# Kernel optimization log

Hardware: AMD Instinct MI355X
Metric: run time of the kernel (lower is better)

The kernel has to match this reference:

```python
import jax, jax.numpy as jnp
import numpy as np

N_SAMPLES = 8192
EMBED_DIM = 128
NUM_CLASSES = 100


def setup_inputs() -> dict:
    key = jax.random.key(0)
    k1, k2 = jax.random.split(key)
    x = jax.random.normal(k1, (N_SAMPLES, EMBED_DIM), dtype=jnp.float32)
    # FastAP assumes L2-normalized embeddings (dist2 = 2 - 2*cos in [0, 4])
    x = x / jnp.linalg.norm(x, axis=1, keepdims=True)
    labels = jax.random.randint(k2, (N_SAMPLES,), 0, NUM_CLASSES, dtype=jnp.int64 if jax.config.jax_enable_x64 else jnp.int32)
    return {"batch": x, "labels": labels, "num_bins": 10}


def reference(batch, labels, num_bins):
    N = batch.shape[0]
    L = num_bins + 1                      # number of histogram bin centers (edges of linspace)
    Delta = 4.0 / num_bins                # bin width
    Z = jnp.linspace(0.0, 4.0, L)

    same = labels[:, None] == labels[None, :]
    eye = jnp.eye(N, dtype=bool)
    I_pos = (same & ~eye).astype(batch.dtype)   # Aff > 0
    I_neg = (~same).astype(batch.dtype)         # Aff < 0 (diag is 'same', so excluded)
    N_pos = I_pos.sum(axis=1)

    # squared euclidean distance for unit-norm rows: 2 - 2*cos
    dist2 = 2.0 - 2.0 * (batch @ batch.T)       # [N, N]

    # soft-binning histogram: one N x N pulse per bin, reduced to per-row counts.
    # lax.map keeps only one [N, N] pulse buffer alive at a time.
    def bin_fn(z):
        pulse = jnp.maximum(0.0, 1.0 - jnp.abs(dist2 - z) / Delta)
        return (jnp.einsum('ij,ij->i', pulse, I_pos),
                jnp.einsum('ij,ij->i', pulse, I_neg))

    hp, hn = jax.lax.map(bin_fn, Z)             # each [L, N]
    h_pos = hp.T                                # [N, L]
    h_neg = hn.T

    H_pos = jnp.cumsum(h_pos, axis=1)
    H = jnp.cumsum(h_pos + h_neg, axis=1)

    # FastAP = h_pos * H_pos / H, with NaN/Inf (H == 0) zeroed, as in the original
    safe_H = jnp.where(H > 0, H, 1.0)
    ap = jnp.where(H > 0, h_pos * H_pos / safe_H, 0.0).sum(axis=1)

    # divide by N_pos; rows with no positives are dropped from the mean
    valid = N_pos > 0
    safe_Np = jnp.where(valid, N_pos, 1.0)
    ap = jnp.where(valid, ap / safe_Np, 0.0)

    n_valid = valid.sum().astype(batch.dtype)
    loss = 1.0 - ap.sum() / n_valid
    return loss
```

## Files before the change

### kernel.cpp

```cpp
#include <hip/hip_runtime.h>

#define NS 8192
#define EMBED 128
#define ROWCHUNK 512
#define NPANEL (ROWCHUNK / 32)
#define AROW 12
#define INV64K (1.0f / 65536.0f)
#define NCLS 100
#define NCAP 160

typedef __bf16 bf16x8 __attribute__((ext_vector_type(8)));
typedef float f32x4 __attribute__((ext_vector_type(4)));
typedef float f32x2 __attribute__((ext_vector_type(2)));
typedef const __attribute__((address_space(1))) unsigned ag_u32;
typedef __attribute__((address_space(3))) unsigned al_u32;

#define OFF_XB  0u
#define OFF_GS  2097152u
#define OFF_GA  4194304u
#define OFF_POS 4587520u
#define OFF_AC  4980736u
#define ZERO_BYTES 786448u

__device__ inline unsigned short f2bf(float f) {
  unsigned u = __float_as_uint(f);
  u += 0x7fffu + ((u >> 16) & 1u);
  return (unsigned short)(u >> 16);
}
__device__ inline float clamp01(float x) { return __builtin_amdgcn_fmed3f(x, 0.f, 1.f); }

__global__ __launch_bounds__(256) void prep_kernel(const float* __restrict__ x,
                                                   unsigned short* __restrict__ xb,
                                                   uint4* __restrict__ zbase) {
  const int gid = blockIdx.x * 256 + threadIdx.x;
  const int row = gid >> 4, g = gid & 15;
  const float4 v0 = reinterpret_cast<const float4*>(x)[row * 32 + g * 2];
  const float4 v1 = reinterpret_cast<const float4*>(x)[row * 32 + g * 2 + 1];
  uint4 o;
  o.x = (unsigned)f2bf(v0.x) | ((unsigned)f2bf(v0.y) << 16);
  o.y = (unsigned)f2bf(v0.z) | ((unsigned)f2bf(v0.w) << 16);
  o.z = (unsigned)f2bf(v1.x) | ((unsigned)f2bf(v1.y) << 16);
  o.w = (unsigned)f2bf(v1.z) | ((unsigned)f2bf(v1.w) << 16);
  reinterpret_cast<uint4*>(xb)[row * 16 + (g ^ (row & 7))] = o;
  if (gid < (int)(ZERO_BYTES / 16u)) zbase[gid] = make_uint4(0u, 0u, 0u, 0u);
}

__global__ __launch_bounds__(256, 8) void fastap_main_kernel(
    const unsigned short* __restrict__ xb,
    const int* __restrict__ labels,
    float* __restrict__ gS, unsigned* __restrict__ gA,
    float* __restrict__ gPos) {
  __shared__ __align__(16) unsigned short sA[2][32 * 128];
  __shared__ int sList[NCAP];
  __shared__ int sCnt;

  const int tid  = threadIdx.x;
  const int wave = tid >> 6;
  const int lane = tid & 63;
  const int l16  = lane & 15;
  const int quad = lane >> 4;

  if (blockIdx.y == NS / ROWCHUNK) {
    if (blockIdx.x >= NCLS) return;
    const int cls = blockIdx.x;

    if (tid == 0) sCnt = 0;
    __syncthreads();
    for (int base = wave * 64; base < NS; base += 256) {
      const int lab = labels[base + lane];
      const unsigned long long m = __ballot(lab == cls);
      if (m) {
        const int fl = (int)__builtin_ctzll(m);
        int wb = 0;
        if (lane == fl) wb = atomicAdd(&sCnt, (int)__popcll(m));
        wb = __shfl(wb, fl, 64);
        if (lab == cls) {
          const int rank = (int)__popcll(m & ((1ull << lane) - 1ull));
          const int idx = wb + rank;
          if (idx < NCAP) sList[idx] = base + lane;
        }
      }
    }
    __syncthreads();
    const int nc = min(sCnt, NCAP);

    for (int cT = wave * 16; cT < nc; cT += 64) {
      const int sc = cT + l16;
      const int Rc = sList[(sc < nc) ? sc : cT];
      bf16x8 bfr[4];
      #pragma unroll
      for (int kb = 0; kb < 4; ++kb) {
        const int pg = (kb * 4 + quad) ^ (Rc & 7);
        bfr[kb] = *reinterpret_cast<const bf16x8*>(&xb[Rc * 128 + pg * 8]);
      }

      f32x2 Hp0 = {0.f, 0.f}, Hp1 = {0.f, 0.f}, Hp2 = {0.f, 0.f};
      f32x2 Hp3 = {0.f, 0.f}, Hp4 = {0.f, 0.f};
      float Hp10 = 0.f;

      for (int rT = 0; rT < nc; rT += 16) {
        const int rl = rT + l16;
        const int Rr = sList[(rl < nc) ? rl : rT];
        f32x4 acc = {0.f, 0.f, 0.f, 0.f};
        #pragma unroll
        for (int kb = 0; kb < 4; ++kb) {
          const int pg = (kb * 4 + quad) ^ (Rr & 7);
          const bf16x8 afr =
              *reinterpret_cast<const bf16x8*>(&xb[Rr * 128 + pg * 8]);
          acc = __builtin_amdgcn_mfma_f32_16x16x32_bf16(afr, bfr[kb], acc, 0, 0, 0);
        }
        #pragma unroll
        for (int r = 0; r < 4; ++r) {
          const int row = rT + quad * 4 + r;
          if (row == sc || row >= nc) continue;
          const float a = acc[r];
          const f32x2 av = {a, a};
          f32x2 t;
          t = __builtin_elementwise_fma(av, (f32x2){5.f, 5.f}, (f32x2){-4.f, -3.f});
          Hp0 += (f32x2){clamp01(t.x), clamp01(t.y)};
          t = __builtin_elementwise_fma(av, (f32x2){5.f, 5.f}, (f32x2){-2.f, -1.f});
          Hp1 += (f32x2){clamp01(t.x), clamp01(t.y)};
          t = __builtin_elementwise_fma(av, (f32x2){5.f, 5.f}, (f32x2){0.f, 1.f});
          Hp2 += (f32x2){clamp01(t.x), clamp01(t.y)};
          t = __builtin_elementwise_fma(av, (f32x2){5.f, 5.f}, (f32x2){2.f, 3.f});
          Hp3 += (f32x2){clamp01(t.x), clamp01(t.y)};
          t = __builtin_elementwise_fma(av, (f32x2){5.f, 5.f}, (f32x2){4.f, 5.f});
          Hp4 += (f32x2){clamp01(t.x), clamp01(t.y)};
          Hp10 += clamp01(fmaf(a, 5.f, 6.f));
        }
      }

      #pragma unroll
      for (int m = 16; m < 64; m <<= 1) {
        Hp0.x += __shfl_xor(Hp0.x, m, 64); Hp0.y += __shfl_xor(Hp0.y, m, 64);
        Hp1.x += __shfl_xor(Hp1.x, m, 64); Hp1.y += __shfl_xor(Hp1.y, m, 64);
        Hp2.x += __shfl_xor(Hp2.x, m, 64); Hp2.y += __shfl_xor(Hp2.y, m, 64);
        Hp3.x += __shfl_xor(Hp3.x, m, 64); Hp3.y += __shfl_xor(Hp3.y, m, 64);
        Hp4.x += __shfl_xor(Hp4.x, m, 64); Hp4.y += __shfl_xor(Hp4.y, m, 64);
        Hp10  += __shfl_xor(Hp10,  m, 64);
      }

      if (quad == 0 && sc < nc) {
        float4* gp = reinterpret_cast<float4*>(gPos + sList[sc] * 12);
        gp[0] = make_float4(Hp0.x, Hp0.y, Hp1.x, Hp1.y);
        gp[1] = make_float4(Hp2.x, Hp2.y, Hp3.x, Hp3.y);
        gp[2] = make_float4(Hp4.x, Hp4.y, Hp10, (float)(nc - 1));
      }
    }
    return;
  }

  const int colBase  = blockIdx.x * 64;
  const int rowChunk = blockIdx.y * ROWCHUNK;

  const int jcol = colBase + wave * 16 + l16;
  bf16x8 bfr[4];
  #pragma unroll
  for (int kb = 0; kb < 4; ++kb) {
    const int pg = (kb * 4 + quad) ^ (l16 & 7);
    bfr[kb] = *reinterpret_cast<const bf16x8*>(&xb[jcol * 128 + pg * 8]);
  }

  f32x2 C01 = {0.f, 0.f}, C23 = {0.f, 0.f};

  int aOff[4];
  #pragma unroll
  for (int kb = 0; kb < 4; ++kb)
    aOff[kb] = l16 * 128 + (((kb * 4 + quad) ^ (l16 & 7)) << 3);

  const unsigned short* xrb = xb + rowChunk * 128;
  auto stage = [&](int p, int b) {
    const unsigned short* src = xrb + p * (32 * 128);
    __builtin_amdgcn_global_load_lds((ag_u32*)(src + tid * 8),
                                     (al_u32*)(&sA[b][tid * 8]), 16, 0, 0);
    __builtin_amdgcn_global_load_lds((ag_u32*)(src + (tid + 256) * 8),
                                     (al_u32*)(&sA[b][(tid + 256) * 8]), 16, 0, 0);
  };

  auto tile16 = [&](const unsigned short* ap, int lcr) {
    bf16x8 a0 = *reinterpret_cast<const bf16x8*>(&ap[aOff[0]]);
    bf16x8 a1 = *reinterpret_cast<const bf16x8*>(&ap[aOff[1]]);
    bf16x8 a2 = *reinterpret_cast<const bf16x8*>(&ap[aOff[2]]);
    bf16x8 a3 = *reinterpret_cast<const bf16x8*>(&ap[aOff[3]]);
    f32x4 acc = {0.f, 0.f, 0.f, 0.f};
    acc = __builtin_amdgcn_mfma_f32_16x16x32_bf16(a0, bfr[0], acc, 0, 0, 0);
    acc = __builtin_amdgcn_mfma_f32_16x16x32_bf16(a1, bfr[1], acc, 0, 0, 0);
    acc = __builtin_amdgcn_mfma_f32_16x16x32_bf16(a2, bfr[2], acc, 0, 0, 0);
    acc = __builtin_amdgcn_mfma_f32_16x16x32_bf16(a3, bfr[3], acc, 0, 0, 0);

    #pragma unroll
    for (int r = 0; r < 4; ++r) {
      const float a = acc[r];
      const f32x2 av = {a, a};
      f32x2 d01 = __builtin_elementwise_fma(av, (f32x2){5.f, 5.f},
                                            (f32x2){-1.f, 0.f});
      f32x2 d23 = __builtin_elementwise_fma(av, (f32x2){5.f, 5.f},
                                            (f32x2){1.f, 2.f});
      d01 = (f32x2){clamp01(d01.x), clamp01(d01.y)};
      d23 = (f32x2){clamp01(d23.x), clamp01(d23.y)};
      C01 += d01; C23 += d23;
    }

    const float mabs = fmaxf(fmaxf(fabsf(acc[0]), fabsf(acc[1])),
                             fmaxf(fabsf(acc[2]), fabsf(acc[3])));
    if (__builtin_expect(mabs > 0.4f, 0)) {
      #pragma unroll
      for (int r = 0; r < 4; ++r) {
        const float a = acc[r];
        if (fabsf(a) <= 0.4f) continue;
        const int i = rowChunk + lcr + quad * 4 + r;
        const float d0 = clamp01(fmaf(a, 5.f, -1.f));
        const float d1 = clamp01(a * 5.f);
        const float d2 = clamp01(fmaf(a, 5.f, 1.f));
        const float d3 = clamp01(fmaf(a, 5.f, 2.f));
        if (i == jcol) {
          C01 -= (f32x2){d0, d1};  C23 -= (f32x2){d2, d3};
          #pragma unroll
          for (int k = 7; k <= 10; ++k)
            atomicAdd(&gA[jcol * AROW + k], (unsigned)(-65536));
        } else {
          const float t = fmaf(a, -5.f, 5.f);
          #pragma unroll
          for (int k = 0; k <= 2; ++k) {
            const float v = clamp01((float)(k + 1) - t);
            const int q = (int)(v * 65536.f + 0.5f);
            if (q) atomicAdd(&gA[jcol * AROW + k], (unsigned)q);
          }
          #pragma unroll
          for (int k = 7; k <= 10; ++k) {
            const float v = clamp01((float)(k + 1) - t) - 1.f;
            const int q = (int)(v * 65536.f - 0.5f);
            if (q) atomicAdd(&gA[jcol * AROW + k], (unsigned)q);
          }
        }
      }
    }
  };

  stage(0, 0);
  __syncthreads();

  #pragma unroll 1
  for (int p = 0; p < NPANEL; ++p) {
    const int cur = p & 1;
    if (p + 1 < NPANEL) stage(p + 1, cur ^ 1);
    tile16(&sA[cur][0],        p * 32);
    tile16(&sA[cur][16 * 128], p * 32 + 16);
    __syncthreads();
  }

  #pragma unroll
  for (int m = 16; m < 64; m <<= 1) {
    C01.x += __shfl_xor(C01.x, m, 64); C01.y += __shfl_xor(C01.y, m, 64);
    C23.x += __shfl_xor(C23.x, m, 64); C23.y += __shfl_xor(C23.y, m, 64);
  }

  if (quad == 0) {
    const int slot = blockIdx.y;
    const float4 cv = make_float4(C01.x, C01.y, C23.x, C23.y);
    reinterpret_cast<float4*>(gS)[slot * NS + jcol] = cv;
  }
}

__global__ __launch_bounds__(256) void epilogue_kernel(
    const float* __restrict__ gS, const unsigned* __restrict__ gA,
    const float* __restrict__ gPos,
    float* __restrict__ accum, unsigned* __restrict__ done,
    float* __restrict__ out) {
  const int i = blockIdx.x * 256 + threadIdx.x;
  const float4* gS4 = reinterpret_cast<const float4*>(gS);
  float4 Cs = make_float4(0.f, 0.f, 0.f, 0.f);
  #pragma unroll 4
  for (int c = 0; c < 16; ++c) {
    const float4 u = gS4[c * NS + i];
    Cs.x += u.x; Cs.y += u.y; Cs.z += u.z; Cs.w += u.w;
  }
  const float CsA[4] = {Cs.x, Cs.y, Cs.z, Cs.w};

  const float4* gp4 = reinterpret_cast<const float4*>(gPos + i * 12);
  const float4 h0 = gp4[0], h1 = gp4[1], h2 = gp4[2];
  const float Hp[11] = {h0.x, h0.y, h0.z, h0.w, h1.x, h1.y,
                        h1.z, h1.w, h2.x, h2.y, h2.z};
  const int np = (int)h2.w;

  float ap = 0.f, val = 0.f, HpPrev = 0.f;
  #pragma unroll
  for (int b = 0; b <= 10; ++b) {
    const float baseH = (b < 3) ? 0.f : (b < 7) ? CsA[b - 3] : 8192.f;
    const float H = baseH + (float)(int)gA[i * AROW + b] * INV64K;
    const float hp = Hp[b] - HpPrev;
    HpPrev = Hp[b];
    if (H > 1e-6f) ap += hp * Hp[b] / H;
  }
  if (np > 0) { ap /= (float)np; val = 1.f; } else ap = 0.f;

  __shared__ float sa[256], sv[256];
  sa[threadIdx.x] = ap; sv[threadIdx.x] = val;
  __syncthreads();
  for (int s = 128; s > 0; s >>= 1) {
    if (threadIdx.x < s) {
      sa[threadIdx.x] += sa[threadIdx.x + s];
      sv[threadIdx.x] += sv[threadIdx.x + s];
    }
    __syncthreads();
  }
  if (threadIdx.x == 0) {
    atomicAdd(&accum[0], sa[0]);
    atomicAdd(&accum[1], sv[0]);
    __threadfence();
    const unsigned prev = atomicAdd(done, 1u);
    if (prev == gridDim.x - 1) {
      const float a = atomicAdd(&accum[0], 0.f);
      const float c = atomicAdd(&accum[1], 0.f);
      out[0] = 1.f - (c > 0.f ? a / c : 0.f);
    }
  }
}

extern "C" void kernel_launch(void* const* d_in, const int* in_sizes, int n_in,
                              void* d_out, int out_size, void* d_ws, size_t ws_size,
                              hipStream_t stream) {
  const float* x      = (const float*)d_in[0];
  const int*   labels = (const int*)d_in[1];
  float* out = (float*)d_out;

  char* ws = (char*)d_ws;
  unsigned short* xb = (unsigned short*)(ws + OFF_XB);
  float*    gS    = (float*)(ws + OFF_GS);
  unsigned* gA    = (unsigned*)(ws + OFF_GA);
  float*    gPos  = (float*)(ws + OFF_POS);
  float*    accum = (float*)(ws + OFF_AC);
  unsigned* done  = (unsigned*)(ws + OFF_AC + 8);

  prep_kernel<<<512, 256, 0, stream>>>(x, xb, (uint4*)(ws + OFF_GA));
  fastap_main_kernel<<<dim3(NS / 64, NS / ROWCHUNK + 1), 256, 0, stream>>>(
      xb, labels, gS, gA, gPos);
  epilogue_kernel<<<NS / 256, 256, 0, stream>>>(gS, gA, gPos, accum, done, out);
}
```

Baseline: 107.6 us.

## Retile waves to 2x2 MFMA tiles sharing A fragments across two column groups

```diff
diff --git a/kernel.cpp b/kernel.cpp
--- a/kernel.cpp
+++ b/kernel.cpp
@@ -17,9 +17,9 @@
 
 #define OFF_XB  0u
 #define OFF_GS  2097152u
-#define OFF_GA  4194304u
-#define OFF_POS 4587520u
-#define OFF_AC  4980736u
+#define OFF_GA  6291456u
+#define OFF_POS 6684672u
+#define OFF_AC  7077888u
 #define ZERO_BYTES 786448u
 
 __device__ inline unsigned short f2bf(float f) {
@@ -150,23 +150,32 @@
     return;
   }
 
+  const int w2   = wave >> 1;
+  const int wr   = wave & 1;
   const int colBase  = blockIdx.x * 64;
   const int rowChunk = blockIdx.y * ROWCHUNK;
 
-  const int jcol = colBase + wave * 16 + l16;
-  bf16x8 bfr[4];
+  bf16x8 bfr[2][4];
+  int jcolv[2];
   #pragma unroll
-  for (int kb = 0; kb < 4; ++kb) {
-    const int pg = (kb * 4 + quad) ^ (l16 & 7);
-    bfr[kb] = *reinterpret_cast<const bf16x8*>(&xb[jcol * 128 + pg * 8]);
-  }
-
-  f32x2 C01 = {0.f, 0.f}, C23 = {0.f, 0.f};
+  for (int s = 0; s < 2; ++s) {
+    const int jc = colBase + w2 * 32 + s * 16 + l16;
+    jcolv[s] = jc;
+    #pragma unroll
+    for (int kb = 0; kb < 4; ++kb) {
+      const int pg = (kb * 4 + quad) ^ (l16 & 7);
+      bfr[s][kb] = *reinterpret_cast<const bf16x8*>(&xb[jc * 128 + pg * 8]);
+    }
+  }
+
+  f32x2 C01[2], C23[2];
+  C01[0] = (f32x2){0.f, 0.f}; C23[0] = (f32x2){0.f, 0.f};
+  C01[1] = (f32x2){0.f, 0.f}; C23[1] = (f32x2){0.f, 0.f};
 
   int aOff[4];
   #pragma unroll
   for (int kb = 0; kb < 4; ++kb)
-    aOff[kb] = l16 * 128 + (((kb * 4 + quad) ^ (l16 & 7)) << 3);
+    aOff[kb] = (wr * 16 + l16) * 128 + (((kb * 4 + quad) ^ (l16 & 7)) << 3);
 
   const unsigned short* xrb = xb + rowChunk * 128;
   auto stage = [&](int p, int b) {
@@ -177,60 +186,74 @@
                                      (al_u32*)(&sA[b][(tid + 256) * 8]), 16, 0, 0);
   };
 
-  auto tile16 = [&](const unsigned short* ap, int lcr) {
+  auto panel32 = [&](const unsigned short* ap, int p) {
     bf16x8 a0 = *reinterpret_cast<const bf16x8*>(&ap[aOff[0]]);
     bf16x8 a1 = *reinterpret_cast<const bf16x8*>(&ap[aOff[1]]);
     bf16x8 a2 = *reinterpret_cast<const bf16x8*>(&ap[aOff[2]]);
     bf16x8 a3 = *reinterpret_cast<const bf16x8*>(&ap[aOff[3]]);
-    f32x4 acc = {0.f, 0.f, 0.f, 0.f};
-    acc = __builtin_amdgcn_mfma_f32_16x16x32_bf16(a0, bfr[0], acc, 0, 0, 0);
-    acc = __builtin_amdgcn_mfma_f32_16x16x32_bf16(a1, bfr[1], acc, 0, 0, 0);
-    acc = __builtin_amdgcn_mfma_f32_16x16x32_bf16(a2, bfr[2], acc, 0, 0, 0);
-    acc = __builtin_amdgcn_mfma_f32_16x16x32_bf16(a3, bfr[3], acc, 0, 0, 0);
+    f32x4 acc0 = {0.f, 0.f, 0.f, 0.f};
+    f32x4 acc1 = {0.f, 0.f, 0.f, 0.f};
+    acc0 = __builtin_amdgcn_mfma_f32_16x16x32_bf16(a0, bfr[0][0], acc0, 0, 0, 0);
+    acc1 = __builtin_amdgcn_mfma_f32_16x16x32_bf16(a0, bfr[1][0], acc1, 0, 0, 0);
+    acc0 = __builtin_amdgcn_mfma_f32_16x16x32_bf16(a1, bfr[0][1], acc0, 0, 0, 0);
+    acc1 = __builtin_amdgcn_mfma_f32_16x16x32_bf16(a1, bfr[1][1], acc1, 0, 0, 0);
+    acc0 = __builtin_amdgcn_mfma_f32_16x16x32_bf16(a2, bfr[0][2], acc0, 0, 0, 0);
+    acc1 = __builtin_amdgcn_mfma_f32_16x16x32_bf16(a2, bfr[1][2], acc1, 0, 0, 0);
+    acc0 = __builtin_amdgcn_mfma_f32_16x16x32_bf16(a3, bfr[0][3], acc0, 0, 0, 0);
+    acc1 = __builtin_amdgcn_mfma_f32_16x16x32_bf16(a3, bfr[1][3], acc1, 0, 0, 0);
 
     #pragma unroll
     for (int r = 0; r < 4; ++r) {
-      const float a = acc[r];
-      const f32x2 av = {a, a};
-      f32x2 d01 = __builtin_elementwise_fma(av, (f32x2){5.f, 5.f},
-                                            (f32x2){-1.f, 0.f});
-      f32x2 d23 = __builtin_elementwise_fma(av, (f32x2){5.f, 5.f},
-                                            (f32x2){1.f, 2.f});
-      d01 = (f32x2){clamp01(d01.x), clamp01(d01.y)};
-      d23 = (f32x2){clamp01(d23.x), clamp01(d23.y)};
-      C01 += d01; C23 += d23;
-    }
-
-    const float mabs = fmaxf(fmaxf(fabsf(acc[0]), fabsf(acc[1])),
-                             fmaxf(fabsf(acc[2]), fabsf(acc[3])));
-    if (__builtin_expect(mabs > 0.4f, 0)) {
       #pragma unroll
-      for (int r = 0; r < 4; ++r) {
-        const float a = acc[r];
-        if (fabsf(a) <= 0.4f) continue;
-        const int i = rowChunk + lcr + quad * 4 + r;
-        const float d0 = clamp01(fmaf(a, 5.f, -1.f));
-        const float d1 = clamp01(a * 5.f);
-        const float d2 = clamp01(fmaf(a, 5.f, 1.f));
-        const float d3 = clamp01(fmaf(a, 5.f, 2.f));
-        if (i == jcol) {
-          C01 -= (f32x2){d0, d1};  C23 -= (f32x2){d2, d3};
-          #pragma unroll
-          for (int k = 7; k <= 10; ++k)
-            atomicAdd(&gA[jcol * AROW + k], (unsigned)(-65536));
-        } else {
-          const float t = fmaf(a, -5.f, 5.f);
-          #pragma unroll
-          for (int k = 0; k <= 2; ++k) {
-            const float v = clamp01((float)(k + 1) - t);
-            const int q = (int)(v * 65536.f + 0.5f);
-            if (q) atomicAdd(&gA[jcol * AROW + k], (unsigned)q);
-          }
-          #pragma unroll
-          for (int k = 7; k <= 10; ++k) {
-            const float v = clamp01((float)(k + 1) - t) - 1.f;
-            const int q = (int)(v * 65536.f - 0.5f);
-            if (q) atomicAdd(&gA[jcol * AROW + k], (unsigned)q);
+      for (int s = 0; s < 2; ++s) {
+        const float a = (s == 0) ? acc0[r] : acc1[r];
+        const f32x2 av = {a, a};
+        f32x2 d01 = __builtin_elementwise_fma(av, (f32x2){5.f, 5.f},
+                                              (f32x2){-1.f, 0.f});
+        f32x2 d23 = __builtin_elementwise_fma(av, (f32x2){5.f, 5.f},
+                                              (f32x2){1.f, 2.f});
+        d01 = (f32x2){clamp01(d01.x), clamp01(d01.y)};
+        d23 = (f32x2){clamp01(d23.x), clamp01(d23.y)};
+        C01[s] += d01; C23[s] += d23;
+      }
+    }
+
+    const float m0 = fmaxf(fmaxf(fabsf(acc0[0]), fabsf(acc0[1])),
+                           fmaxf(fabsf(acc0[2]), fabsf(acc0[3])));
+    const float m1 = fmaxf(fmaxf(fabsf(acc1[0]), fabsf(acc1[1])),
+                           fmaxf(fabsf(acc1[2]), fabsf(acc1[3])));
+    if (__builtin_expect(fmaxf(m0, m1) > 0.4f, 0)) {
+      #pragma unroll
+      for (int s = 0; s < 2; ++s) {
+        #pragma unroll
+        for (int r = 0; r < 4; ++r) {
+          const float a = (s == 0) ? acc0[r] : acc1[r];
+          if (fabsf(a) <= 0.4f) continue;
+          const int i = rowChunk + p * 32 + wr * 16 + quad * 4 + r;
+          const int jc = jcolv[s];
+          const float d0 = clamp01(fmaf(a, 5.f, -1.f));
+          const float d1 = clamp01(a * 5.f);
+          const float d2 = clamp01(fmaf(a, 5.f, 1.f));
+          const float d3 = clamp01(fmaf(a, 5.f, 2.f));
+          if (i == jc) {
+            C01[s] -= (f32x2){d0, d1};  C23[s] -= (f32x2){d2, d3};
+            #pragma unroll
+            for (int k = 7; k <= 10; ++k)
+              atomicAdd(&gA[jc * AROW + k], (unsigned)(-65536));
+          } else {
+            const float t = fmaf(a, -5.f, 5.f);
+            #pragma unroll
+            for (int k = 0; k <= 2; ++k) {
+              const float v = clamp01((float)(k + 1) - t);
+              const int q = (int)(v * 65536.f + 0.5f);
+              if (q) atomicAdd(&gA[jc * AROW + k], (unsigned)q);
+            }
+            #pragma unroll
+            for (int k = 7; k <= 10; ++k) {
+              const float v = clamp01((float)(k + 1) - t) - 1.f;
+              const int q = (int)(v * 65536.f - 0.5f);
+              if (q) atomicAdd(&gA[jc * AROW + k], (unsigned)q);
+            }
           }
         }
       }
@@ -244,21 +267,28 @@
   for (int p = 0; p < NPANEL; ++p) {
     const int cur = p & 1;
     if (p + 1 < NPANEL) stage(p + 1, cur ^ 1);
-    tile16(&sA[cur][0],        p * 32);
-    tile16(&sA[cur][16 * 128], p * 32 + 16);
+    panel32(&sA[cur][0], p);
     __syncthreads();
   }
 
   #pragma unroll
   for (int m = 16; m < 64; m <<= 1) {
-    C01.x += __shfl_xor(C01.x, m, 64); C01.y += __shfl_xor(C01.y, m, 64);
-    C23.x += __shfl_xor(C23.x, m, 64); C23.y += __shfl_xor(C23.y, m, 64);
+    #pragma unroll
+    for (int s = 0; s < 2; ++s) {
+      C01[s].x += __shfl_xor(C01[s].x, m, 64);
+      C01[s].y += __shfl_xor(C01[s].y, m, 64);
+      C23[s].x += __shfl_xor(C23[s].x, m, 64);
+      C23[s].y += __shfl_xor(C23[s].y, m, 64);
+    }
   }
 
   if (quad == 0) {
-    const int slot = blockIdx.y;
-    const float4 cv = make_float4(C01.x, C01.y, C23.x, C23.y);
-    reinterpret_cast<float4*>(gS)[slot * NS + jcol] = cv;
+    const int slot = blockIdx.y * 2 + wr;
+    #pragma unroll
+    for (int s = 0; s < 2; ++s) {
+      const float4 cv = make_float4(C01[s].x, C01[s].y, C23[s].x, C23[s].y);
+      reinterpret_cast<float4*>(gS)[slot * NS + jcolv[s]] = cv;
+    }
   }
 }
 
@@ -270,8 +300,8 @@
   const int i = blockIdx.x * 256 + threadIdx.x;
   const float4* gS4 = reinterpret_cast<const float4*>(gS);
   float4 Cs = make_float4(0.f, 0.f, 0.f, 0.f);
-  #pragma unroll 4
-  for (int c = 0; c < 16; ++c) {
+  #pragma unroll 8
+  for (int c = 0; c < 32; ++c) {
     const float4 u = gS4[c * NS + i];
     Cs.x += u.x; Cs.y += u.y; Cs.z += u.z; Cs.w += u.w;
   }
```

Result: slower. 117.0 us (+8.7%).
